# Performance work log

Hardware: AMD Instinct MI355X
Metric: run time of the kernel (lower is better)

## Reference

```python
import jax, jax.numpy as jnp
import numpy as np

# Module constants derived from default grid_config
D = 59          # depth bins: (60-1)/1
C_OUT = 64
X, Y, Z = 128, 128, 7
STRIDE = 16
GRID_LB = np.array([-51.2, -51.2, -2.5], dtype=np.float32)
GRID_IV = np.array([0.8, 0.8, 1.0], dtype=np.float32)
D0, DSTEP = 1.0, 1.0

B, N, C_IN, H, W = 4, 6, 256, 16, 44


def _voxel_coords():
    xs, ys, zs = np.meshgrid(np.arange(X), np.arange(Y), np.arange(Z), indexing='ij')
    coords = np.stack([xs, ys, zs], axis=-1).reshape(-1, 3).astype(np.float32)
    coords = coords * GRID_IV + GRID_LB  # [V, 3] ego-frame voxel centers
    return coords


def _camera_rig(rng):
    """Realistic 6-camera rig: yawed cameras looking outward, z_cam = forward."""
    c2e = np.zeros((B, N, 4, 4), dtype=np.float32)
    K = np.zeros((B, N, 3, 3), dtype=np.float32)
    for b in range(B):
        for n in range(N):
            a = 2.0 * np.pi * n / N + 0.02 * rng.standard_normal()
            f = np.array([np.cos(a), np.sin(a), 0.0])           # camera forward (z_cam)
            x_cam = np.array([-np.sin(a), np.cos(a), 0.0])      # camera right
            y_cam = np.array([0.0, 0.0, -1.0])                   # camera down
            R = np.stack([x_cam, y_cam, f], axis=1)              # columns = cam axes in ego
            t = 1.0 * f + np.array([0.0, 0.0, 1.5])
            c2e[b, n, :3, :3] = R
            c2e[b, n, :3, 3] = t
            c2e[b, n, 3, 3] = 1.0
            fl = 400.0 + 5.0 * rng.standard_normal()
            K[b, n] = np.array([[fl, 0.0, 352.0], [0.0, fl, 128.0], [0.0, 0.0, 1.0]])
    return c2e, K


def setup_inputs() -> dict:
    key = jax.random.key(0)
    k1, k2, k3 = jax.random.split(key, 3)
    img_feats = jax.random.normal(k1, (B, N, C_IN, H, W), dtype=jnp.float32)
    c2e, K = _camera_rig(np.random.default_rng(0))
    # depth_net: 1x1 conv in_channels -> D + C_OUT
    w_depth = jax.random.normal(k2, (D + C_OUT, C_IN), dtype=jnp.float32) * (1.0 / np.sqrt(C_IN))
    b_depth = jax.random.normal(k3, (D + C_OUT,), dtype=jnp.float32) * 0.01
    return {
        'img_feats': img_feats,
        'cam2ego': jnp.asarray(c2e),
        'cam_intrinsics': jnp.asarray(K),
        'w_depth': w_depth,
        'b_depth': b_depth,
    }


def reference(img_feats, cam2ego, cam_intrinsics, w_depth, b_depth):
    Bc, Nc, C, Hc, Wc = img_feats.shape
    # 1x1 conv == per-pixel linear
    x = jnp.einsum('bnchw,oc->bnhwo', img_feats, w_depth) + b_depth  # [B,N,H,W,D+C_OUT]
    depth = jax.nn.softmax(x[..., :D], axis=-1)                      # [B,N,H,W,D]
    feat = x[..., D:]                                                # [B,N,H,W,C_OUT]

    vox = jnp.asarray(_voxel_coords())                               # [V,3]
    V = vox.shape[0]
    vox_h = jnp.concatenate([vox, jnp.ones((V, 1), vox.dtype)], axis=1)  # [V,4]

    e2c = jnp.linalg.inv(cam2ego)                                    # [B,N,4,4]
    cam = jnp.einsum('bnij,vj->bnvi', e2c, vox_h)[..., :3]           # [B,N,V,3]
    z = cam[..., 2]
    z_safe = jnp.maximum(z, 0.1)
    norm = cam[..., :2] / z_safe[..., None]
    homo = jnp.concatenate([norm, jnp.ones_like(z[..., None])], axis=-1)  # [B,N,V,3]
    img = jnp.einsum('bnij,bnvj->bnvi', cam_intrinsics, homo)[..., :2]
    fc = img / STRIDE                                                # feature-plane coords

    depth_bin = ((z - D0) / DSTEP).astype(jnp.int32)                 # trunc toward 0, matches .long()
    valid = (
        (fc[..., 0] >= 0) & (fc[..., 0] < Wc)
        & (fc[..., 1] >= 0) & (fc[..., 1] < Hc)
        & (z > 0.5)
        & (depth_bin >= 0) & (depth_bin < D)
    )

    u = jnp.clip(fc[..., 0].astype(jnp.int32), 0, Wc - 1)            # [B,N,V]
    v = jnp.clip(fc[..., 1].astype(jnp.int32), 0, Hc - 1)
    d = jnp.clip(depth_bin, 0, D - 1)
    hw = v * Wc + u

    feat_flat = feat.reshape(Bc, Nc, Hc * Wc, C_OUT)
    sampled_feat = jnp.take_along_axis(feat_flat, hw[..., None], axis=2)   # [B,N,V,C_OUT]
    depth_flat = depth.reshape(Bc, Nc, Hc * Wc * D)
    sampled_depth = jnp.take_along_axis(depth_flat, hw * D + d, axis=2)    # [B,N,V]

    wgt = sampled_depth * valid.astype(sampled_depth.dtype)
    # scatter_add at flat_idx == voxel index (identity) -> masked sum over cameras
    bev = jnp.einsum('bnv,bnvc->bvc', wgt, sampled_feat)             # [B,V,C_OUT]
    bev = bev.reshape(Bc, X, Y, Z, C_OUT).sum(axis=3)                # collapse Z
    bev = bev.transpose(0, 3, 2, 1)                                  # [B,C_OUT,Y,X]
    return bev, depth
```

## Files before the change

### kernel.cpp

```cpp
#include <hip/hip_runtime.h>
#include <math.h>

#define D_BINS 59
#define CO     64
#define CI     256
#define NB     4
#define NC     6
#define H_IMG  16
#define W_IMG  44
#define HW     704
#define NPIX   (NB*NC*HW)
#define XD     128
#define YD     128
#define ZD     7
#define NOUT   123

__global__ void k_inv(const float* __restrict__ c2e, float* __restrict__ e2c) {
    int i = threadIdx.x;
    if (i >= NB * NC) return;
    const float* M = c2e + i * 16;
    double a = M[0], b = M[1], c = M[2], t0 = M[3];
    double d = M[4], e = M[5], f = M[6], t1 = M[7];
    double g = M[8], h = M[9], ii = M[10], t2 = M[11];
    double A00 = e*ii - f*h, A01 = c*h - b*ii, A02 = b*f - c*e;
    double A10 = f*g - d*ii, A11 = a*ii - c*g, A12 = c*d - a*f;
    double A20 = d*h - e*g,  A21 = b*g - a*h,  A22 = a*e - b*d;
    double det = a*A00 + b*A10 + c*A20;
    double inv = 1.0 / det;
    double r00 = A00*inv, r01 = A01*inv, r02 = A02*inv;
    double r10 = A10*inv, r11 = A11*inv, r12 = A12*inv;
    double r20 = A20*inv, r21 = A21*inv, r22 = A22*inv;
    double s0 = -(r00*t0 + r01*t1 + r02*t2);
    double s1 = -(r10*t0 + r11*t1 + r12*t2);
    double s2 = -(r20*t0 + r21*t1 + r22*t2);
    float* o = e2c + i * 12;
    o[0] = (float)r00; o[1] = (float)r01; o[2]  = (float)r02; o[3]  = (float)s0;
    o[4] = (float)r10; o[5] = (float)r11; o[6]  = (float)r12; o[7]  = (float)s1;
    o[8] = (float)r20; o[9] = (float)r21; o[10] = (float)r22; o[11] = (float)s2;
}

__global__ __launch_bounds__(256) void k_head(
    const float* __restrict__ img, const float* __restrict__ wd,
    const float* __restrict__ bd, float* __restrict__ depth_out,
    float* __restrict__ feat_ws) {
    __shared__ float smem[5376];
    float* A_lds = smem;
    float* W_lds = smem + 1152;

    const int tid = threadIdx.x;
    const int ti = tid & 7;
    const int tj = tid >> 3;
    const int p0 = blockIdx.x * 32;
    const int bn = p0 / HW;
    const int hw0 = p0 % HW;
    const float* imgb = img + (size_t)bn * CI * HW + hw0;

    float acc[4][4];
#pragma unroll
    for (int i = 0; i < 4; ++i)
#pragma unroll
        for (int j = 0; j < 4; ++j) acc[i][j] = 0.f;

    for (int kc = 0; kc < 8; ++kc) {
        {
            int r = tid >> 3, c4 = tid & 7;
            float4 v = *(const float4*)(imgb + (size_t)(kc * 32 + r) * HW + c4 * 4);
            float* dst = A_lds + r * 36 + c4 * 4;
            *(float4*)dst = v;
        }
#pragma unroll
        for (int it = 0; it < 4; ++it) {
            int idx = tid + it * 256;
            int o = idx >> 3, c4 = idx & 7;
            float4 v = make_float4(0.f, 0.f, 0.f, 0.f);
            if (o < NOUT) v = *(const float4*)(wd + (size_t)o * CI + kc * 32 + c4 * 4);
            W_lds[(c4 * 4 + 0) * 132 + o] = v.x;
            W_lds[(c4 * 4 + 1) * 132 + o] = v.y;
            W_lds[(c4 * 4 + 2) * 132 + o] = v.z;
            W_lds[(c4 * 4 + 3) * 132 + o] = v.w;
        }
        __syncthreads();
#pragma unroll
        for (int k = 0; k < 32; ++k) {
            float4 a = *(const float4*)(A_lds + k * 36 + ti * 4);
            float4 w = *(const float4*)(W_lds + k * 132 + tj * 4);
            float av[4] = {a.x, a.y, a.z, a.w};
            float wv[4] = {w.x, w.y, w.z, w.w};
#pragma unroll
            for (int i = 0; i < 4; ++i)
#pragma unroll
                for (int j = 0; j < 4; ++j)
                    acc[i][j] = fmaf(av[i], wv[j], acc[i][j]);
        }
        __syncthreads();
    }

    float* X = smem;
    float bias[4];
#pragma unroll
    for (int j = 0; j < 4; ++j) {
        int o = tj * 4 + j;
        bias[j] = (o < NOUT) ? bd[o] : 0.f;
    }
#pragma unroll
    for (int i = 0; i < 4; ++i) {
        int px = ti * 4 + i;
#pragma unroll
        for (int j = 0; j < 4; ++j) {
            int o = tj * 4 + j;
            if (o < NOUT) X[px * 124 + o] = acc[i][j] + bias[j];
        }
    }
    __syncthreads();

    {
        int px = tid >> 3, q = tid & 7;
        const float* src = X + px * 124 + D_BINS + q * 8;
        float* dst = feat_ws + (size_t)(p0 + px) * CO + q * 8;
#pragma unroll
        for (int m = 0; m < 8; ++m) dst[m] = src[m];
    }

    if (tid < 32) {
        int px = tid;
        float* row = X + px * 124;
        float m = row[0];
        for (int o = 1; o < D_BINS; ++o) m = fmaxf(m, row[o]);
        float s = 0.f;
        for (int o = 0; o < D_BINS; ++o) {
            float e = __expf(row[o] - m);
            row[o] = e;
            s += e;
        }
        float* dout = depth_out + (size_t)(p0 + px) * D_BINS;
        for (int o = 0; o < D_BINS; ++o) dout[o] = row[o] / s;
    }
}

__global__ __launch_bounds__(256) void k_splat(
    const float* __restrict__ e2c, const float* __restrict__ Kmat,
    const float* __restrict__ depth_g, const float* __restrict__ feat_ws,
    float* __restrict__ bev) {
    const int tx = threadIdx.x;
    const int cq = threadIdx.y;
    const int x = blockIdx.x * 64 + tx;
    const int y = blockIdx.y;
    const int b = blockIdx.z;
    const float wx = (float)x * 0.8f + (-51.2f);
    const float wy = (float)y * 0.8f + (-51.2f);

    float acc[16];
#pragma unroll
    for (int m = 0; m < 16; ++m) acc[m] = 0.f;

    for (int n = 0; n < NC; ++n) {
        const int bn = b * NC + n;
        const float* E = e2c + bn * 12;
        const float* Km = Kmat + bn * 9;
        const float k00 = Km[0], k01 = Km[1], k02 = Km[2];
        const float k10 = Km[3], k11 = Km[4], k12 = Km[5];
        const float e02 = E[2], e12 = E[6], e22 = E[10];
        const float bx0 = E[0] * wx + E[1] * wy + E[3];
        const float bx1 = E[4] * wx + E[5] * wy + E[7];
        const float bx2 = E[8] * wx + E[9] * wy + E[11];
#pragma unroll
        for (int z = 0; z < ZD; ++z) {
            const float wz = -2.5f + (float)z;
            const float cx = bx0 + e02 * wz;
            const float cy = bx1 + e12 * wz;
            const float cz = bx2 + e22 * wz;
            const float zs = fmaxf(cz, 0.1f);
            const float rz = 1.0f / zs;
            const float xn = cx * rz;
            const float yn = cy * rz;
            const float fu = (k00 * xn + k01 * yn + k02) * 0.0625f;
            const float fv = (k10 * xn + k11 * yn + k12) * 0.0625f;
            const int bin = (int)(cz - 1.0f);
            const bool valid = (fu >= 0.f) & (fu < (float)W_IMG) &
                               (fv >= 0.f) & (fv < (float)H_IMG) &
                               (cz > 0.5f) & (bin >= 0) & (bin < D_BINS);
            if (valid) {
                int u = (int)fu; u = u < 0 ? 0 : (u > W_IMG - 1 ? W_IMG - 1 : u);
                int v = (int)fv; v = v < 0 ? 0 : (v > H_IMG - 1 ? H_IMG - 1 : v);
                int hw = v * W_IMG + u;
                float wgt = depth_g[((size_t)bn * HW + hw) * D_BINS + bin];
                const float4* fp =
                    (const float4*)(feat_ws + ((size_t)bn * HW + hw) * CO + cq * 16);
                float4 f0 = fp[0], f1 = fp[1], f2 = fp[2], f3 = fp[3];
                acc[0]  = fmaf(wgt, f0.x, acc[0]);
                acc[1]  = fmaf(wgt, f0.y, acc[1]);
                acc[2]  = fmaf(wgt, f0.z, acc[2]);
                acc[3]  = fmaf(wgt, f0.w, acc[3]);
                acc[4]  = fmaf(wgt, f1.x, acc[4]);
                acc[5]  = fmaf(wgt, f1.y, acc[5]);
                acc[6]  = fmaf(wgt, f1.z, acc[6]);
                acc[7]  = fmaf(wgt, f1.w, acc[7]);
                acc[8]  = fmaf(wgt, f2.x, acc[8]);
                acc[9]  = fmaf(wgt, f2.y, acc[9]);
                acc[10] = fmaf(wgt, f2.z, acc[10]);
                acc[11] = fmaf(wgt, f2.w, acc[11]);
                acc[12] = fmaf(wgt, f3.x, acc[12]);
                acc[13] = fmaf(wgt, f3.y, acc[13]);
                acc[14] = fmaf(wgt, f3.z, acc[14]);
                acc[15] = fmaf(wgt, f3.w, acc[15]);
            }
        }
    }
    float* ob = bev + (((size_t)b * CO + cq * 16) * YD + y) * XD + x;
#pragma unroll
    for (int m = 0; m < 16; ++m) ob[(size_t)m * YD * XD] = acc[m];
}

extern "C" void kernel_launch(void* const* d_in, const int* in_sizes, int n_in,
                              void* d_out, int out_size, void* d_ws, size_t ws_size,
                              hipStream_t stream) {
    const float* img  = (const float*)d_in[0];
    const float* c2e  = (const float*)d_in[1];
    const float* Kmat = (const float*)d_in[2];
    const float* wd   = (const float*)d_in[3];
    const float* bd   = (const float*)d_in[4];
    float* bev = (float*)d_out;
    float* depth_out = bev + (size_t)NB * CO * YD * XD;
    float* feat_ws = (float*)d_ws;
    float* e2c = feat_ws + (size_t)NPIX * CO;

    k_inv<<<1, 64, 0, stream>>>(c2e, e2c);
    k_head<<<NPIX / 32, 256, 0, stream>>>(img, wd, bd, depth_out, feat_ws);
    k_splat<<<dim3(2, YD, NB), dim3(64, 4, 1), 0, stream>>>(e2c, Kmat, depth_out,
                                                            feat_ws, bev);
}
```

Baseline: 133.3 us.

## Pre-transpose depth-net weights and restructure head GEMM with wave-uniform weight loads

```diff
diff --git a/kernel.cpp b/kernel.cpp
--- a/kernel.cpp
+++ b/kernel.cpp
@@ -15,10 +15,7 @@
 #define ZD     7
 #define NOUT   123
 
-__global__ void k_inv(const float* __restrict__ c2e, float* __restrict__ e2c) {
-    int i = threadIdx.x;
-    if (i >= NB * NC) return;
-    const float* M = c2e + i * 16;
+__device__ void inv_rigid(const float* __restrict__ M, float* __restrict__ o) {
     double a = M[0], b = M[1], c = M[2], t0 = M[3];
     double d = M[4], e = M[5], f = M[6], t1 = M[7];
     double g = M[8], h = M[9], ii = M[10], t2 = M[11];
@@ -30,100 +27,87 @@
     double r00 = A00*inv, r01 = A01*inv, r02 = A02*inv;
     double r10 = A10*inv, r11 = A11*inv, r12 = A12*inv;
     double r20 = A20*inv, r21 = A21*inv, r22 = A22*inv;
-    double s0 = -(r00*t0 + r01*t1 + r02*t2);
-    double s1 = -(r10*t0 + r11*t1 + r12*t2);
-    double s2 = -(r20*t0 + r21*t1 + r22*t2);
-    float* o = e2c + i * 12;
-    o[0] = (float)r00; o[1] = (float)r01; o[2]  = (float)r02; o[3]  = (float)s0;
-    o[4] = (float)r10; o[5] = (float)r11; o[6]  = (float)r12; o[7]  = (float)s1;
-    o[8] = (float)r20; o[9] = (float)r21; o[10] = (float)r22; o[11] = (float)s2;
-}
-
-__global__ __launch_bounds__(256) void k_head(
-    const float* __restrict__ img, const float* __restrict__ wd,
+    o[0] = (float)r00; o[1] = (float)r01; o[2]  = (float)r02;
+    o[3] = (float)(-(r00*t0 + r01*t1 + r02*t2));
+    o[4] = (float)r10; o[5] = (float)r11; o[6]  = (float)r12;
+    o[7] = (float)(-(r10*t0 + r11*t1 + r12*t2));
+    o[8] = (float)r20; o[9] = (float)r21; o[10] = (float)r22;
+    o[11] = (float)(-(r20*t0 + r21*t1 + r22*t2));
+}
+
+__global__ __launch_bounds__(256) void k_pre(
+    const float* __restrict__ wd, const float* __restrict__ c2e,
+    float* __restrict__ wt, float* __restrict__ e2c) {
+    const int o = blockIdx.x;
+    const int k = threadIdx.x;
+    float v = (o < NOUT) ? wd[(size_t)o * CI + k] : 0.f;
+    wt[(size_t)k * 128 + o] = v;
+    if (blockIdx.x == 0 && k < NB * NC)
+        inv_rigid(c2e + k * 16, e2c + k * 12);
+}
+
+__global__ __launch_bounds__(512) void k_head(
+    const float* __restrict__ img, const float* __restrict__ wt,
     const float* __restrict__ bd, float* __restrict__ depth_out,
     float* __restrict__ feat_ws) {
-    __shared__ float smem[5376];
+    __shared__ float smem[8448 + 64];
     float* A_lds = smem;
-    float* W_lds = smem + 1152;
-
-    const int tid = threadIdx.x;
-    const int ti = tid & 7;
-    const int tj = tid >> 3;
-    const int p0 = blockIdx.x * 32;
+    float* S = smem + 8448;
+
+    const int px = threadIdx.x;
+    const int tid = threadIdx.y * 64 + threadIdx.x;
+    const int o0 = __builtin_amdgcn_readfirstlane(threadIdx.y << 4);
+    const int p0 = blockIdx.x * 64;
     const int bn = p0 / HW;
     const int hw0 = p0 % HW;
     const float* imgb = img + (size_t)bn * CI * HW + hw0;
 
-    float acc[4][4];
-#pragma unroll
-    for (int i = 0; i < 4; ++i)
-#pragma unroll
-        for (int j = 0; j < 4; ++j) acc[i][j] = 0.f;
-
-    for (int kc = 0; kc < 8; ++kc) {
-        {
-            int r = tid >> 3, c4 = tid & 7;
-            float4 v = *(const float4*)(imgb + (size_t)(kc * 32 + r) * HW + c4 * 4);
-            float* dst = A_lds + r * 36 + c4 * 4;
-            *(float4*)dst = v;
-        }
-#pragma unroll
-        for (int it = 0; it < 4; ++it) {
-            int idx = tid + it * 256;
-            int o = idx >> 3, c4 = idx & 7;
-            float4 v = make_float4(0.f, 0.f, 0.f, 0.f);
-            if (o < NOUT) v = *(const float4*)(wd + (size_t)o * CI + kc * 32 + c4 * 4);
-            W_lds[(c4 * 4 + 0) * 132 + o] = v.x;
-            W_lds[(c4 * 4 + 1) * 132 + o] = v.y;
-            W_lds[(c4 * 4 + 2) * 132 + o] = v.z;
-            W_lds[(c4 * 4 + 3) * 132 + o] = v.w;
+    float acc[16];
+#pragma unroll
+    for (int j = 0; j < 16; ++j) acc[j] = 0.f;
+
+    for (int kc = 0; kc < 4; ++kc) {
+#pragma unroll
+        for (int it = 0; it < 2; ++it) {
+            int idx = tid + it * 512;
+            int r = idx >> 4, c4 = idx & 15;
+            float4 v = *(const float4*)(imgb + (size_t)(kc * 64 + r) * HW + c4 * 4);
+            *(float4*)(A_lds + r * 64 + c4 * 4) = v;
         }
         __syncthreads();
-#pragma unroll
-        for (int k = 0; k < 32; ++k) {
-            float4 a = *(const float4*)(A_lds + k * 36 + ti * 4);
-            float4 w = *(const float4*)(W_lds + k * 132 + tj * 4);
-            float av[4] = {a.x, a.y, a.z, a.w};
-            float wv[4] = {w.x, w.y, w.z, w.w};
-#pragma unroll
-            for (int i = 0; i < 4; ++i)
-#pragma unroll
-                for (int j = 0; j < 4; ++j)
-                    acc[i][j] = fmaf(av[i], wv[j], acc[i][j]);
+        const float* wr = wt + (size_t)(kc * 64) * 128 + o0;
+#pragma unroll 4
+        for (int k = 0; k < 64; ++k) {
+            float a = A_lds[k * 64 + px];
+            const float* w = wr + k * 128;
+#pragma unroll
+            for (int j = 0; j < 16; ++j)
+                acc[j] = fmaf(a, w[j], acc[j]);
         }
         __syncthreads();
     }
 
     float* X = smem;
-    float bias[4];
-#pragma unroll
-    for (int j = 0; j < 4; ++j) {
-        int o = tj * 4 + j;
-        bias[j] = (o < NOUT) ? bd[o] : 0.f;
-    }
-#pragma unroll
-    for (int i = 0; i < 4; ++i) {
-        int px = ti * 4 + i;
-#pragma unroll
-        for (int j = 0; j < 4; ++j) {
-            int o = tj * 4 + j;
-            if (o < NOUT) X[px * 124 + o] = acc[i][j] + bias[j];
+#pragma unroll
+    for (int j = 0; j < 16; ++j) {
+        int o = o0 + j;
+        if (o < NOUT) {
+            int col = (o < D_BINS) ? o : o + 5;
+            X[px * 132 + col] = acc[j] + bd[o];
         }
     }
     __syncthreads();
 
-    {
-        int px = tid >> 3, q = tid & 7;
-        const float* src = X + px * 124 + D_BINS + q * 8;
-        float* dst = feat_ws + (size_t)(p0 + px) * CO + q * 8;
-#pragma unroll
-        for (int m = 0; m < 8; ++m) dst[m] = src[m];
-    }
-
-    if (tid < 32) {
-        int px = tid;
-        float* row = X + px * 124;
+#pragma unroll
+    for (int it = 0; it < 2; ++it) {
+        int g = tid + it * 512;
+        int p = g >> 4, m = g & 15;
+        float4 v = *(const float4*)(X + p * 132 + 64 + m * 4);
+        *(float4*)(feat_ws + (size_t)(p0 + p) * CO + m * 4) = v;
+    }
+
+    if (tid < 64) {
+        float* row = X + tid * 132;
         float m = row[0];
         for (int o = 1; o < D_BINS; ++o) m = fmaxf(m, row[o]);
         float s = 0.f;
@@ -132,8 +116,14 @@
             row[o] = e;
             s += e;
         }
-        float* dout = depth_out + (size_t)(p0 + px) * D_BINS;
-        for (int o = 0; o < D_BINS; ++o) dout[o] = row[o] / s;
+        S[tid] = 1.f / s;
+    }
+    __syncthreads();
+
+    for (int g = tid; g < 64 * D_BINS; g += 512) {
+        int p = g / D_BINS;
+        int o = g - p * D_BINS;
+        depth_out[(size_t)p0 * D_BINS + g] = X[p * 132 + o] * S[p];
     }
 }
 
@@ -180,8 +170,8 @@
                                (fv >= 0.f) & (fv < (float)H_IMG) &
                                (cz > 0.5f) & (bin >= 0) & (bin < D_BINS);
             if (valid) {
-                int u = (int)fu; u = u < 0 ? 0 : (u > W_IMG - 1 ? W_IMG - 1 : u);
-                int v = (int)fv; v = v < 0 ? 0 : (v > H_IMG - 1 ? H_IMG - 1 : v);
+                int u = (int)fu;
+                int v = (int)fv;
                 int hw = v * W_IMG + u;
                 float wgt = depth_g[((size_t)bn * HW + hw) * D_BINS + bin];
                 const float4* fp =
@@ -222,10 +212,11 @@
     float* bev = (float*)d_out;
     float* depth_out = bev + (size_t)NB * CO * YD * XD;
     float* feat_ws = (float*)d_ws;
-    float* e2c = feat_ws + (size_t)NPIX * CO;
-
-    k_inv<<<1, 64, 0, stream>>>(c2e, e2c);
-    k_head<<<NPIX / 32, 256, 0, stream>>>(img, wd, bd, depth_out, feat_ws);
+    float* wt  = feat_ws + (size_t)NPIX * CO;
+    float* e2c = wt + 256 * 128;
+
+    k_pre<<<128, 256, 0, stream>>>(wd, c2e, wt, e2c);
+    k_head<<<NPIX / 64, dim3(64, 8, 1), 0, stream>>>(img, wt, bd, depth_out, feat_ws);
     k_splat<<<dim3(2, YD, NB), dim3(64, 4, 1), 0, stream>>>(e2c, Kmat, depth_out,
                                                             feat_ws, bev);
 }
```

New measurement: 130.7 us. Within noise of the previous version (-1.9%).
